# Optimization experiments

Measured on AMD Instinct MI355X. Metric: run time of the kernel, lower is better.

Reference implementation:

```python
import jax, jax.numpy as jnp
import numpy as np

DN = ('NCHW', 'OIHW', 'NCHW')


def conv2d(x, w, b, stride):
    y = jax.lax.conv_general_dilated(x, w, (stride, stride), 'VALID', dimension_numbers=DN)
    return y + b[None, :, None, None]


def split_heads(t, heads):
    # 'B (c h) H W -> B h (H W) c'  (channel index = c*heads + h)
    B, C, H, W = t.shape
    c = C // heads
    t = t.reshape(B, c, heads, H * W)
    return jnp.transpose(t, (0, 2, 3, 1))  # [B, h, HW, c]


def setup_inputs() -> dict:
    key = jax.random.key(0)
    ks = jax.random.split(key, 7)
    B, dim, H, W = 4, 256, 128, 128
    inner, p = 256, 8
    s = 0.02
    return {
        'x':  jax.random.normal(ks[0], (B, dim, H, W), jnp.float32),
        'Wq': jax.random.normal(ks[1], (inner, dim, 1, 1), jnp.float32) * s,
        'bq': jax.random.normal(ks[2], (inner,), jnp.float32) * s,
        'Wk': jax.random.normal(ks[3], (inner, dim, p, p), jnp.float32) * s,
        'bk': jax.random.normal(ks[4], (inner,), jnp.float32) * s,
        'Wv': jax.random.normal(ks[5], (inner, dim, p, p), jnp.float32) * s,
        'bv': jax.random.normal(ks[6], (inner,), jnp.float32) * s,
    }


def reference(x, Wq, bq, Wk, bk, Wv, bv):
    heads = 8
    p = Wk.shape[-1]
    B, C, H, W = x.shape
    q = conv2d(x, Wq, bq, 1)      # [B, inner, H, W]
    k = conv2d(x, Wk, bk, p)      # [B, inner, H/p, W/p]
    v = conv2d(x, Wv, bv, p)
    q = split_heads(q, heads)     # [B, h, HW, c]
    k = split_heads(k, heads)     # [B, h, K, c]
    v = split_heads(v, heads)
    # NOTE: original module applies no 1/sqrt(d) scaling
    dots = jnp.einsum('bhnc,bhkc->bhnk', q, k)
    attn = jax.nn.softmax(dots, axis=-1)
    out = jnp.einsum('bhnk,bhkc->bhnc', attn, v)  # [B, h, HW, c]
    # 'B h (H W) c -> B (c h) H W'
    c = out.shape[-1]
    out = jnp.transpose(out, (0, 3, 1, 2)).reshape(B, c * heads, H, W)
    return out
```

## Files before the change

### kernel.cpp

```cpp
#include <hip/hip_runtime.h>
#include <stdint.h>

typedef short sh4 __attribute__((ext_vector_type(4)));
typedef short short8 __attribute__((ext_vector_type(8)));
typedef float f32x4 __attribute__((ext_vector_type(4)));
typedef float f4 __attribute__((ext_vector_type(4)));
typedef _Float16 half4 __attribute__((ext_vector_type(4)));
typedef _Float16 half8 __attribute__((ext_vector_type(8)));
typedef unsigned int uint2v __attribute__((ext_vector_type(2)));

__device__ __forceinline__ short f2h(float f) {
    _Float16 h = (_Float16)f;
    return __builtin_bit_cast(short, h);
}

__device__ __forceinline__ f32x4 mfma_k32(short8 a, short8 b, f32x4 c) {
    return __builtin_amdgcn_mfma_f32_16x16x32_f16(
        __builtin_bit_cast(half8, a), __builtin_bit_cast(half8, b), c, 0, 0, 0);
}
__device__ __forceinline__ f32x4 mfma_k16(half4 a, half4 b, f32x4 c) {
    return __builtin_amdgcn_mfma_f32_16x16x16f16(a, b, c, 0, 0, 0);
}
__device__ __forceinline__ unsigned int pkrtz(float a, float b) {
    return __builtin_bit_cast(unsigned int, __builtin_amdgcn_cvt_pkrtz(a, b));
}
__device__ __forceinline__ float exp2_raw(float x) {
    float r;
    asm("v_exp_f32 %0, %1" : "=v"(r) : "v"(x));
    return r;
}


__device__ __forceinline__ void transpose64(const float* __restrict__ src,
                                            short* __restrict__ dst,
                                            int srcSlowStride, int dstRowStride) {
    __shared__ float tile[64][65];
    const int t = threadIdx.x;
#pragma unroll
    for (int i = 0; i < 4; ++i) {
        int idx = i * 1024 + t * 4;
        int fast = idx & 63, slow = idx >> 6;
        f4 v = *(const f4*)(src + (long)slow * srcSlowStride + fast);
        tile[slow][fast]     = v[0];
        tile[slow][fast + 1] = v[1];
        tile[slow][fast + 2] = v[2];
        tile[slow][fast + 3] = v[3];
    }
    __syncthreads();
#pragma unroll
    for (int i = 0; i < 2; ++i) {
        int ch = i * 256 + t;
        int fast = ch >> 3, sg = ch & 7;
        short8 v;
#pragma unroll
        for (int j = 0; j < 8; ++j) v[j] = f2h(tile[sg * 8 + j][fast]);
        *(short8*)(dst + (long)fast * dstRowStride + sg * 8) = v;
    }
}

__global__ __launch_bounds__(256) void k_pack_x(const float* __restrict__ x,
                                                short* __restrict__ xn) {
    int bi = blockIdx.x;
    int ct = bi & 3, pxt = (bi >> 2) & 255, b = bi >> 10;
    const float* src = x + (((long)(b * 256 + ct * 64)) << 14) + (long)pxt * 64;
    short* dst = xn + (((long)(b << 14) + pxt * 64) * 256) + ct * 64;
    transpose64(src, dst, 16384, 256);
}

__global__ __launch_bounds__(256) void k_pack_w(const float* __restrict__ wk,
                                                const float* __restrict__ wv,
                                                short* __restrict__ wp) {
    int bi = blockIdx.x;
    int ct = bi & 3, oc = bi >> 2;
    const float* base = (oc < 256) ? (wk + (long)oc * 16384) : (wv + (long)(oc - 256) * 16384);
    const float* src = base + ct * 4096;
    short* dst = wp + (long)oc * 16384 + ct * 64;
    transpose64(src, dst, 64, 256);
}

__global__ __launch_bounds__(256) void k_pack_wq(const float* __restrict__ wq,
                                                 short* __restrict__ wqp) {
    int i = blockIdx.x * 256 + threadIdx.x;
    wqp[i] = f2h(wq[i]);
}

__global__ __launch_bounds__(256) void k_kv_gemm(const short* __restrict__ xn,
                                                 const short* __restrict__ wp,
                                                 float* __restrict__ part) {
    __shared__ short Al[128 * 64];
    __shared__ short Bl[64 * 64];
    int bid = blockIdx.x;
    int wg = (bid & 7) * 64 + (bid >> 3);
    int nb = wg & 7, pm = (wg >> 3) & 7, kc = wg >> 6;
    int t = threadIdx.x, l = t & 63, w = t >> 6;
    int wm = w >> 1, wn = w & 1;
    int low = l & 15, q = l >> 4;

    short* lda[4];
    short* ldb[2];
#pragma unroll
    for (int i = 0; i < 4; ++i) {
        int g = i * 256 + t;
        int row = g >> 3, lg = g & 7;
        lda[i] = Al + row * 64 + ((lg ^ (row & 7)) * 8);
    }
#pragma unroll
    for (int i = 0; i < 2; ++i) {
        int g = i * 256 + t;
        int row = g >> 3, lg = g & 7;
        ldb[i] = Bl + row * 64 + ((lg ^ (row & 7)) * 8);
    }

    f32x4 acc[4][2];
#pragma unroll
    for (int mt = 0; mt < 4; ++mt)
#pragma unroll
        for (int nt = 0; nt < 2; ++nt) acc[mt][nt] = (f32x4){0.f, 0.f, 0.f, 0.f};

#pragma unroll 1
    for (int kk4 = 0; kk4 < 8; ++kk4) {
        const short* apt[4];
        const short* bpt[2];
        int dydx = kc * 8 + kk4;
#pragma unroll
        for (int i = 0; i < 4; ++i) {
            int g = i * 256 + t;
            int row = g >> 3, lg = g & 7;
            int patch = pm * 128 + row;
            int bb = patch >> 8, pid = patch & 255;
            int ph = pid >> 4, pw = pid & 15;
            int px = (ph * 8 + (dydx >> 3)) * 128 + pw * 8 + (dydx & 7);
            apt[i] = xn + ((long)(bb << 14) + px) * 256 + lg * 8;
        }
#pragma unroll
        for (int i = 0; i < 2; ++i) {
            int g = i * 256 + t;
            int row = g >> 3, lg = g & 7;
            int oc = nb * 64 + row;
            bpt[i] = wp + (long)oc * 16384 + kc * 2048 + kk4 * 256 + lg * 8;
        }
#pragma unroll
        for (int j = 0; j < 4; ++j) {
            short8 va[4], vb[2];
#pragma unroll
            for (int i = 0; i < 4; ++i) va[i] = *(const short8*)(apt[i] + j * 64);
#pragma unroll
            for (int i = 0; i < 2; ++i) vb[i] = *(const short8*)(bpt[i] + j * 64);
#pragma unroll
            for (int i = 0; i < 4; ++i) *(short8*)lda[i] = va[i];
#pragma unroll
            for (int i = 0; i < 2; ++i) *(short8*)ldb[i] = vb[i];
            __syncthreads();
#pragma unroll
            for (int ks = 0; ks < 2; ++ks) {
                short8 af[4], bf[2];
#pragma unroll
                for (int mt = 0; mt < 4; ++mt) {
                    int row = wm * 64 + mt * 16 + low;
                    int lg = ks * 4 + q;
                    af[mt] = *(const short8*)(Al + row * 64 + ((lg ^ (row & 7)) * 8));
                }
#pragma unroll
                for (int nt = 0; nt < 2; ++nt) {
                    int row = wn * 32 + nt * 16 + low;
                    int lg = ks * 4 + q;
                    bf[nt] = *(const short8*)(Bl + row * 64 + ((lg ^ (row & 7)) * 8));
                }
#pragma unroll
                for (int mt = 0; mt < 4; ++mt)
#pragma unroll
                    for (int nt = 0; nt < 2; ++nt)
                        acc[mt][nt] = mfma_k32(af[mt], bf[nt], acc[mt][nt]);
            }
            __syncthreads();
        }
    }
#pragma unroll
    for (int mt = 0; mt < 4; ++mt) {
        int patch = pm * 128 + wm * 64 + mt * 16 + q * 4;
#pragma unroll
        for (int nt = 0; nt < 2; ++nt) {
            int oc = nb * 64 + wn * 32 + nt * 16 + low;
#pragma unroll
            for (int r = 0; r < 4; ++r)
                part[((long)kc * 1024 + patch + r) * 512 + oc] = acc[mt][nt][r];
        }
    }
}

__global__ __launch_bounds__(256) void k_kv_fin(const float* __restrict__ part,
                                                const float* __restrict__ bk,
                                                const float* __restrict__ bv,
                                                short* __restrict__ kp,
                                                short* __restrict__ vp) {
    int idx = blockIdx.x * 256 + threadIdx.x;
    int oc = idx & 511, patch = idx >> 9;
    float s = 0.f;
#pragma unroll
    for (int kc = 0; kc < 8; ++kc) s += part[(long)kc * 524288 + idx];
    int b = patch >> 8, key = patch & 255;
    if (oc < 256) {
        s += bk[oc];
        kp[(((long)(b * 8 + (oc & 7)) * 256) + key) * 32 + (oc >> 3)] = f2h(s);
    } else {
        int o = oc - 256;
        s += bv[o];
        vp[(((long)(b * 8 + (o & 7)) * 32) + (o >> 3)) * 256 + key] = f2h(s);
    }
}

__global__ __launch_bounds__(256) void k_q_gemm(const short* __restrict__ xn,
                                                const short* __restrict__ wqp,
                                                const float* __restrict__ bq,
                                                short* __restrict__ qp) {
    __shared__ short Tb[64 * 256];
    int bi = blockIdx.x;
    int b = bi >> 8, tile = bi & 255;
    long px0 = (long)tile * 64;
    int t = threadIdx.x, l = t & 63, w = t >> 6;
    int low = l & 15, q = l >> 4;

    const short* xb = xn + (((long)(b << 14)) + px0) * 256;

    float bqv[4];
#pragma unroll
    for (int nt = 0; nt < 4; ++nt) bqv[nt] = bq[w * 64 + nt * 16 + low];

    f32x4 acc[4][4];
#pragma unroll
    for (int mt = 0; mt < 4; ++mt)
#pragma unroll
        for (int nt = 0; nt < 4; ++nt) acc[mt][nt] = (f32x4){0.f, 0.f, 0.f, 0.f};

#pragma unroll
    for (int kstep = 0; kstep < 8; ++kstep) {
        short8 af[4], bf[4];
#pragma unroll
        for (int mt = 0; mt < 4; ++mt)
            af[mt] = *(const short8*)(xb + (mt * 16 + low) * 256 + kstep * 32 + q * 8);
#pragma unroll
        for (int nt = 0; nt < 4; ++nt)
            bf[nt] = *(const short8*)(wqp + (w * 64 + nt * 16 + low) * 256 + kstep * 32 + q * 8);
#pragma unroll
        for (int mt = 0; mt < 4; ++mt)
#pragma unroll
            for (int nt = 0; nt < 4; ++nt)
                acc[mt][nt] = mfma_k32(af[mt], bf[nt], acc[mt][nt]);
    }
    const float LOG2E = 1.44269504088896f;
#pragma unroll
    for (int mt = 0; mt < 4; ++mt)
#pragma unroll
        for (int nt = 0; nt < 4; ++nt) {
            int oc = w * 64 + nt * 16 + low;
            int h8 = oc & 7, cc = oc >> 3;
            int gi = h8 * 4 + (cc >> 3);
#pragma unroll
            for (int r = 0; r < 4; ++r) {
                int px = mt * 16 + q * 4 + r;
                Tb[px * 256 + ((gi ^ (px & 7)) * 8) + (cc & 7)] =
                    f2h((acc[mt][nt][r] + bqv[nt]) * LOG2E);
            }
        }
    __syncthreads();
#pragma unroll
    for (int i = 0; i < 8; ++i) {
        int g = i * 256 + t;
        int pxl = g >> 5, g16 = g & 31;
        int hh = g16 >> 2, oct = g16 & 3;
        short8 v = *(const short8*)(Tb + pxl * 256 + ((g16 ^ (pxl & 7)) * 8));
        *(short8*)(qp + (((long)(b * 8 + hh) * 16384) + px0 + pxl) * 32 + oct * 8) = v;
    }
}

__global__ __launch_bounds__(256) void k_attn(const short* __restrict__ qp,
                                              const short* __restrict__ kp,
                                              const short* __restrict__ vp,
                                              float* __restrict__ out) {
    __shared__ short Vl[32 * 264];
    int bi = blockIdx.x;
    int tile = bi & 63, h = (bi >> 6) & 7, b = bi >> 9;
    int bh = b * 8 + h;
    long px0 = (long)tile * 256;
    int t = threadIdx.x, l = t & 63, w = t >> 6;
    int low = l & 15, q = l >> 4;

    const short* kbase = kp + (long)bh * 8192;
    const short* vbase = vp + (long)bh * 8192;
    const short* qbase = qp + (long)bh * 16384 * 32;

#pragma unroll
    for (int i = 0; i < 4; ++i) {
        int g = i * 256 + t;
        int c = g >> 5, k8 = g & 31;
        *(short8*)(Vl + c * 264 + k8 * 8) = *(const short8*)(vbase + c * 256 + k8 * 8);
    }
    short8 kf[16];
#pragma unroll
    for (int mt = 0; mt < 16; ++mt)
        kf[mt] = *(const short8*)(kbase + (mt * 16 + low) * 32 + q * 8);
    __syncthreads();

    const short* vA = Vl + low * 264 + q * 4;
    const sh4 sone = {0x3C00, 0x3C00, 0x3C00, 0x3C00};
    const half4 vones = __builtin_bit_cast(half4, sone);

#pragma unroll 1
    for (int nt = 0; nt < 4; ++nt) {
        long px = px0 + w * 64 + nt * 16 + low;
        short8 bq2 = *(const short8*)(qbase + px * 32 + q * 8);

        f32x4 dd[16];
        float m = -1e30f;
#pragma unroll
        for (int mt = 0; mt < 16; ++mt) {
            dd[mt] = mfma_k32(kf[mt], bq2, (f32x4){0.f, 0.f, 0.f, 0.f});
            m = fmaxf(fmaxf(dd[mt][0], dd[mt][1]), m);
            m = fmaxf(fmaxf(dd[mt][2], dd[mt][3]), m);
        }
        m = fmaxf(m, __shfl_xor(m, 16));
        m = fmaxf(m, __shfl_xor(m, 32));

        uint2v pk[16];
#pragma unroll
        for (int mt = 0; mt < 16; ++mt) {
            float p0 = exp2_raw(dd[mt][0] - m);
            float p1 = exp2_raw(dd[mt][1] - m);
            float p2 = exp2_raw(dd[mt][2] - m);
            float p3 = exp2_raw(dd[mt][3] - m);
            pk[mt][0] = pkrtz(p0, p1);
            pk[mt][1] = pkrtz(p2, p3);
        }

        f32x4 o2[2], os;
        o2[0] = (f32x4){0.f, 0.f, 0.f, 0.f};
        o2[1] = (f32x4){0.f, 0.f, 0.f, 0.f};
        os    = (f32x4){0.f, 0.f, 0.f, 0.f};
        __builtin_amdgcn_s_setprio(1);
#pragma unroll
        for (int kc = 0; kc < 16; ++kc) {
            half4 pb = __builtin_bit_cast(half4, pk[kc]);
            half4 av0 = __builtin_bit_cast(half4, *(const sh4*)(vA + kc * 16));
            half4 av1 = __builtin_bit_cast(half4, *(const sh4*)(vA + 4224 + kc * 16));
            o2[0] = mfma_k16(av0, pb, o2[0]);
            o2[1] = mfma_k16(av1, pb, o2[1]);
            os    = mfma_k16(vones, pb, os);
        }
        __builtin_amdgcn_s_setprio(0);
        float inv = 1.0f / os[0];

#pragma unroll
        for (int ct = 0; ct < 2; ++ct)
#pragma unroll
            for (int r = 0; r < 4; ++r) {
                int c = ct * 16 + q * 4 + r;
                out[(((long)(b * 256 + c * 8 + h)) << 14) + px] = o2[ct][r] * inv;
            }
    }
}

extern "C" void kernel_launch(void* const* d_in, const int* in_sizes, int n_in,
                              void* d_out, int out_size, void* d_ws, size_t ws_size,
                              hipStream_t stream) {
    const float* x  = (const float*)d_in[0];
    const float* Wq = (const float*)d_in[1];
    const float* bq = (const float*)d_in[2];
    const float* Wk = (const float*)d_in[3];
    const float* bk = (const float*)d_in[4];
    const float* Wv = (const float*)d_in[5];
    const float* bv = (const float*)d_in[6];
    float* out = (float*)d_out;

    char* ws = (char*)d_ws;
    const size_t OFF_XN = 0;
    const size_t OFF_Q  = 33554432;
    const size_t OFF_WP = 67108864;
    const size_t OFF_WQ = 83886080;
    const size_t OFF_KP = 84017152;
    const size_t OFF_VP = 84541440;
    const size_t OFF_PT = 85065728;
    const size_t NEEDED = 118620160;
    if (ws_size < NEEDED) return;

    short* xn  = (short*)(ws + OFF_XN);
    short* qp  = (short*)(ws + OFF_Q);
    short* wp  = (short*)(ws + OFF_WP);
    short* wqp = (short*)(ws + OFF_WQ);
    short* kp  = (short*)(ws + OFF_KP);
    short* vp  = (short*)(ws + OFF_VP);
    float* part= (float*)(ws + OFF_PT);

    k_pack_x <<<dim3(4096), dim3(256), 0, stream>>>(x, xn);
    k_pack_w <<<dim3(2048), dim3(256), 0, stream>>>(Wk, Wv, wp);
    k_pack_wq<<<dim3(256),  dim3(256), 0, stream>>>(Wq, wqp);
    k_kv_gemm<<<dim3(512),  dim3(256), 0, stream>>>(xn, wp, part);
    k_kv_fin <<<dim3(2048), dim3(256), 0, stream>>>(part, bk, bv, kp, vp);
    k_q_gemm <<<dim3(1024), dim3(256), 0, stream>>>(xn, wqp, bq, qp);
    k_attn   <<<dim3(2048), dim3(256), 0, stream>>>(qp, kp, vp, out);
}
```

Baseline: 143.0 us.

## Merge pack kernels and co-schedule KV and Q GEMMs in one launch

Combines the three packing kernels into a single launch that dispatches by block index, and merges the KV conv GEMM and the Q projection GEMM into one kernel whose blocks are interleaved two Q to one KV. The goal is to cut launch overhead and tail effects, and to let the long split-K KV blocks overlap with the short Q blocks on the compute units. Shared memory is unified at 32KB per block, so Q blocks now reserve the same LDS as KV blocks, which may affect occupancy.

Result: slower. 150.2 us (+5.0%).

```diff
diff --git a/kernel.cpp b/kernel.cpp
--- a/kernel.cpp
+++ b/kernel.cpp
@@ -33,8 +33,8 @@
 
 __device__ __forceinline__ void transpose64(const float* __restrict__ src,
                                             short* __restrict__ dst,
-                                            int srcSlowStride, int dstRowStride) {
-    __shared__ float tile[64][65];
+                                            int srcSlowStride, int dstRowStride,
+                                            float (*tile)[65]) {
     const int t = threadIdx.x;
 #pragma unroll
     for (int i = 0; i < 4; ++i) {
@@ -58,38 +58,42 @@
     }
 }
 
-__global__ __launch_bounds__(256) void k_pack_x(const float* __restrict__ x,
-                                                short* __restrict__ xn) {
-    int bi = blockIdx.x;
-    int ct = bi & 3, pxt = (bi >> 2) & 255, b = bi >> 10;
-    const float* src = x + (((long)(b * 256 + ct * 64)) << 14) + (long)pxt * 64;
-    short* dst = xn + (((long)(b << 14) + pxt * 64) * 256) + ct * 64;
-    transpose64(src, dst, 16384, 256);
-}
-
-__global__ __launch_bounds__(256) void k_pack_w(const float* __restrict__ wk,
-                                                const float* __restrict__ wv,
-                                                short* __restrict__ wp) {
-    int bi = blockIdx.x;
-    int ct = bi & 3, oc = bi >> 2;
-    const float* base = (oc < 256) ? (wk + (long)oc * 16384) : (wv + (long)(oc - 256) * 16384);
-    const float* src = base + ct * 4096;
-    short* dst = wp + (long)oc * 16384 + ct * 64;
-    transpose64(src, dst, 64, 256);
-}
-
-__global__ __launch_bounds__(256) void k_pack_wq(const float* __restrict__ wq,
-                                                 short* __restrict__ wqp) {
-    int i = blockIdx.x * 256 + threadIdx.x;
-    wqp[i] = f2h(wq[i]);
-}
-
-__global__ __launch_bounds__(256) void k_kv_gemm(const short* __restrict__ xn,
-                                                 const short* __restrict__ wp,
-                                                 float* __restrict__ part) {
-    __shared__ short Al[128 * 64];
-    __shared__ short Bl[64 * 64];
+__global__ __launch_bounds__(256) void k_pack_all(const float* __restrict__ x,
+                                                  const float* __restrict__ wk,
+                                                  const float* __restrict__ wv,
+                                                  const float* __restrict__ wq,
+                                                  short* __restrict__ xn,
+                                                  short* __restrict__ wp,
+                                                  short* __restrict__ wqp) {
+    __shared__ float tile[64][65];
     int bid = blockIdx.x;
+    if (bid < 4096) {
+        int bi = bid;
+        int ct = bi & 3, pxt = (bi >> 2) & 255, b = bi >> 10;
+        const float* src = x + (((long)(b * 256 + ct * 64)) << 14) + (long)pxt * 64;
+        short* dst = xn + (((long)(b << 14) + pxt * 64) * 256) + ct * 64;
+        transpose64(src, dst, 16384, 256, tile);
+    } else if (bid < 6144) {
+        int bi = bid - 4096;
+        int ct = bi & 3, oc = bi >> 2;
+        const float* base = (oc < 256) ? (wk + (long)oc * 16384)
+                                       : (wv + (long)(oc - 256) * 16384);
+        const float* src = base + ct * 4096;
+        short* dst = wp + (long)oc * 16384 + ct * 64;
+        transpose64(src, dst, 64, 256, tile);
+    } else {
+        int i = (bid - 6144) * 256 + threadIdx.x;
+        wqp[i] = f2h(wq[i]);
+    }
+}
+
+
+__device__ __forceinline__ void kv_gemm_body(const short* __restrict__ xn,
+                                             const short* __restrict__ wp,
+                                             float* __restrict__ part,
+                                             int bid, short* smem) {
+    short* Al = smem;
+    short* Bl = smem + 8192;
     int wg = (bid & 7) * 64 + (bid >> 3);
     int nb = wg & 7, pm = (wg >> 3) & 7, kc = wg >> 6;
     int t = threadIdx.x, l = t & 63, w = t >> 6;
@@ -186,6 +190,83 @@
                 part[((long)kc * 1024 + patch + r) * 512 + oc] = acc[mt][nt][r];
         }
     }
+}
+
+__device__ __forceinline__ void q_gemm_body(const short* __restrict__ xn,
+                                            const short* __restrict__ wqp,
+                                            const float* __restrict__ bq,
+                                            short* __restrict__ qp,
+                                            int bi, short* smem) {
+    short* Tb = smem;
+    int b = bi >> 8, tile = bi & 255;
+    long px0 = (long)tile * 64;
+    int t = threadIdx.x, l = t & 63, w = t >> 6;
+    int low = l & 15, q = l >> 4;
+
+    const short* xb = xn + (((long)(b << 14)) + px0) * 256;
+
+    float bqv[4];
+#pragma unroll
+    for (int nt = 0; nt < 4; ++nt) bqv[nt] = bq[w * 64 + nt * 16 + low];
+
+    f32x4 acc[4][4];
+#pragma unroll
+    for (int mt = 0; mt < 4; ++mt)
+#pragma unroll
+        for (int nt = 0; nt < 4; ++nt) acc[mt][nt] = (f32x4){0.f, 0.f, 0.f, 0.f};
+
+#pragma unroll
+    for (int kstep = 0; kstep < 8; ++kstep) {
+        short8 af[4], bf[4];
+#pragma unroll
+        for (int mt = 0; mt < 4; ++mt)
+            af[mt] = *(const short8*)(xb + (mt * 16 + low) * 256 + kstep * 32 + q * 8);
+#pragma unroll
+        for (int nt = 0; nt < 4; ++nt)
+            bf[nt] = *(const short8*)(wqp + (w * 64 + nt * 16 + low) * 256 + kstep * 32 + q * 8);
+#pragma unroll
+        for (int mt = 0; mt < 4; ++mt)
+#pragma unroll
+            for (int nt = 0; nt < 4; ++nt)
+                acc[mt][nt] = mfma_k32(af[mt], bf[nt], acc[mt][nt]);
+    }
+    const float LOG2E = 1.44269504088896f;
+#pragma unroll
+    for (int mt = 0; mt < 4; ++mt)
+#pragma unroll
+        for (int nt = 0; nt < 4; ++nt) {
+            int oc = w * 64 + nt * 16 + low;
+            int h8 = oc & 7, cc = oc >> 3;
+            int gi = h8 * 4 + (cc >> 3);
+#pragma unroll
+            for (int r = 0; r < 4; ++r) {
+                int px = mt * 16 + q * 4 + r;
+                Tb[px * 256 + ((gi ^ (px & 7)) * 8) + (cc & 7)] =
+                    f2h((acc[mt][nt][r] + bqv[nt]) * LOG2E);
+            }
+        }
+    __syncthreads();
+#pragma unroll
+    for (int i = 0; i < 8; ++i) {
+        int g = i * 256 + t;
+        int pxl = g >> 5, g16 = g & 31;
+        int hh = g16 >> 2, oct = g16 & 3;
+        short8 v = *(const short8*)(Tb + pxl * 256 + ((g16 ^ (pxl & 7)) * 8));
+        *(short8*)(qp + (((long)(b * 8 + hh) * 16384) + px0 + pxl) * 32 + oct * 8) = v;
+    }
+}
+
+__global__ __launch_bounds__(256) void k_gemm_all(const short* __restrict__ xn,
+                                                  const short* __restrict__ wp,
+                                                  const short* __restrict__ wqp,
+                                                  const float* __restrict__ bq,
+                                                  float* __restrict__ part,
+                                                  short* __restrict__ qp) {
+    __shared__ __attribute__((aligned(16))) short smem[16384];
+    int bid = blockIdx.x;
+    int k3 = bid / 3, r3 = bid - k3 * 3;
+    if (r3 == 2) kv_gemm_body(xn, wp, part, k3, smem);
+    else         q_gemm_body(xn, wqp, bq, qp, k3 * 2 + r3, smem);
 }
 
 __global__ __launch_bounds__(256) void k_kv_fin(const float* __restrict__ part,
@@ -206,70 +287,6 @@
         int o = oc - 256;
         s += bv[o];
         vp[(((long)(b * 8 + (o & 7)) * 32) + (o >> 3)) * 256 + key] = f2h(s);
-    }
-}
-
-__global__ __launch_bounds__(256) void k_q_gemm(const short* __restrict__ xn,
-                                                const short* __restrict__ wqp,
-                                                const float* __restrict__ bq,
-                                                short* __restrict__ qp) {
-    __shared__ short Tb[64 * 256];
-    int bi = blockIdx.x;
-    int b = bi >> 8, tile = bi & 255;
-    long px0 = (long)tile * 64;
-    int t = threadIdx.x, l = t & 63, w = t >> 6;
-    int low = l & 15, q = l >> 4;
-
-    const short* xb = xn + (((long)(b << 14)) + px0) * 256;
-
-    float bqv[4];
-#pragma unroll
-    for (int nt = 0; nt < 4; ++nt) bqv[nt] = bq[w * 64 + nt * 16 + low];
-
-    f32x4 acc[4][4];
-#pragma unroll
-    for (int mt = 0; mt < 4; ++mt)
-#pragma unroll
-        for (int nt = 0; nt < 4; ++nt) acc[mt][nt] = (f32x4){0.f, 0.f, 0.f, 0.f};
-
-#pragma unroll
-    for (int kstep = 0; kstep < 8; ++kstep) {
-        short8 af[4], bf[4];
-#pragma unroll
-        for (int mt = 0; mt < 4; ++mt)
-            af[mt] = *(const short8*)(xb + (mt * 16 + low) * 256 + kstep * 32 + q * 8);
-#pragma unroll
-        for (int nt = 0; nt < 4; ++nt)
-            bf[nt] = *(const short8*)(wqp + (w * 64 + nt * 16 + low) * 256 + kstep * 32 + q * 8);
-#pragma unroll
-        for (int mt = 0; mt < 4; ++mt)
-#pragma unroll
-            for (int nt = 0; nt < 4; ++nt)
-                acc[mt][nt] = mfma_k32(af[mt], bf[nt], acc[mt][nt]);
-    }
-    const float LOG2E = 1.44269504088896f;
-#pragma unroll
-    for (int mt = 0; mt < 4; ++mt)
-#pragma unroll
-        for (int nt = 0; nt < 4; ++nt) {
-            int oc = w * 64 + nt * 16 + low;
-            int h8 = oc & 7, cc = oc >> 3;
-            int gi = h8 * 4 + (cc >> 3);
-#pragma unroll
-            for (int r = 0; r < 4; ++r) {
-                int px = mt * 16 + q * 4 + r;
-                Tb[px * 256 + ((gi ^ (px & 7)) * 8) + (cc & 7)] =
-                    f2h((acc[mt][nt][r] + bqv[nt]) * LOG2E);
-            }
-        }
-    __syncthreads();
-#pragma unroll
-    for (int i = 0; i < 8; ++i) {
-        int g = i * 256 + t;
-        int pxl = g >> 5, g16 = g & 31;
-        int hh = g16 >> 2, oct = g16 & 3;
-        short8 v = *(const short8*)(Tb + pxl * 256 + ((g16 ^ (pxl & 7)) * 8));
-        *(short8*)(qp + (((long)(b * 8 + hh) * 16384) + px0 + pxl) * 32 + oct * 8) = v;
     }
 }
 
@@ -390,11 +407,8 @@
     short* vp  = (short*)(ws + OFF_VP);
     float* part= (float*)(ws + OFF_PT);
 
-    k_pack_x <<<dim3(4096), dim3(256), 0, stream>>>(x, xn);
-    k_pack_w <<<dim3(2048), dim3(256), 0, stream>>>(Wk, Wv, wp);
-    k_pack_wq<<<dim3(256),  dim3(256), 0, stream>>>(Wq, wqp);
-    k_kv_gemm<<<dim3(512),  dim3(256), 0, stream>>>(xn, wp, part);
-    k_kv_fin <<<dim3(2048), dim3(256), 0, stream>>>(part, bk, bv, kp, vp);
-    k_q_gemm <<<dim3(1024), dim3(256), 0, stream>>>(xn, wqp, bq, qp);
-    k_attn   <<<dim3(2048), dim3(256), 0, stream>>>(qp, kp, vp, out);
-}
+    k_pack_all<<<dim3(6400), dim3(256), 0, stream>>>(x, Wk, Wv, Wq, xn, wp, wqp);
+    k_gemm_all<<<dim3(1536), dim3(256), 0, stream>>>(xn, wp, wqp, bq, part, qp);
+    k_kv_fin  <<<dim3(2048), dim3(256), 0, stream>>>(part, bk, bv, kp, vp);
+    k_attn    <<<dim3(2048), dim3(256), 0, stream>>>(qp, kp, vp, out);
+}
```
